# Performance work log

Hardware: AMD Instinct MI355X
Metric: run time of the kernel (lower is better)

## Reference

```python
import jax, jax.numpy as jnp
import numpy as np

N_NODES = 100000
N_EDGES = 3200000
D_IN = 96      # sum(latent_dim)
D_OUT = 32     # latent_dim[-1]
N_HEADS = 4
LEAKY_SLOPE = 0.2


def setup_inputs() -> dict:
    key = jax.random.key(0)
    k_x, k_w, k_a, k_src, k_dst = jax.random.split(key, 5)
    x = jax.random.normal(k_x, (N_NODES, D_IN), dtype=jnp.float32)
    # per-head GAT params (xavier-ish scale)
    W = jax.random.normal(k_w, (N_HEADS, D_IN, D_OUT), dtype=jnp.float32) * (1.414 / np.sqrt(D_IN))
    a = jax.random.normal(k_a, (N_HEADS, 2 * D_OUT), dtype=jnp.float32) * 0.1
    edge_src = jax.random.randint(k_src, (N_EDGES,), 0, N_NODES)
    edge_dst = jax.random.randint(k_dst, (N_EDGES,), 0, N_NODES)
    return {"x": x, "W": W, "a": a, "edge_src": edge_src, "edge_dst": edge_dst}


def reference(x, W, a, edge_src, edge_dst):
    # Multi-head sparse GAT layer (SpGraphAttentionLayer, concat=True, eval mode).
    N = x.shape[0]
    n_heads, _, d_out = W.shape
    outs = []
    for i in range(n_heads):  # small fixed head loop; data dims fully vectorized
        h = x @ W[i]                                   # [N, d_out]
        # a @ cat(h[src], h[dst]) == h[src]@a1 + h[dst]@a2 (avoids [E, 2*d_out] concat)
        s = h[edge_src] @ a[i, :d_out] + h[edge_dst] @ a[i, d_out:]   # [E]
        edge_e = jnp.exp(-jax.nn.leaky_relu(s, LEAKY_SLOPE))          # [E]
        # sparse_coo(edge, edge_e, [N,N]) @ h  ==  scatter-add of edge_e * h[dst] into src
        msg = edge_e[:, None] * h[edge_dst]                           # [E, d_out]
        h_prime = jax.ops.segment_sum(msg, edge_src, num_segments=N)  # [N, d_out]
        outs.append(jax.nn.elu(h_prime))
    return jnp.concatenate(outs, axis=1)  # [N, n_heads * d_out]
```

## Files before the change

### kernel.cpp

```cpp
#include <hip/hip_runtime.h>
#include <hip/hip_bf16.h>

#define DIN 96
#define DOUT 32
#define NH 4
#define DTOT 128
#define SLOPE 0.2f
#define NPBF 64
#define BSH 7
#define BNODES 128
#define MAXB 1024
#define EPB 16384

__device__ __forceinline__ unsigned int packbf2(float lo, float hi) {
    unsigned int a = __float_as_uint(lo), b = __float_as_uint(hi);
    a += 0x7fffu + ((a >> 16) & 1u);
    b += 0x7fffu + ((b >> 16) & 1u);
    return (a >> 16) | (b & 0xffff0000u);
}

__global__ __launch_bounds__(256) void feat_kernel(
    const float* __restrict__ x, const float* __restrict__ W,
    const float* __restrict__ a,
    unsigned int* __restrict__ hq,
    float2* __restrict__ usrc, float2* __restrict__ vdst,
    int* __restrict__ counts, int n_nodes)
{
    __shared__ float Wlo[DIN * 64];
    __shared__ float Whi[DIN * 64];
    __shared__ float al[NH * 2 * DOUT];
    const int t = threadIdx.x;

    if (blockIdx.x == 0)
        for (int i = t; i < MAXB; i += 256) counts[i] = 0;

    for (int i = t; i < DIN * DTOT; i += 256) {
        int k = i >> 7, c = i & 127;
        int head = c >> 5, j = c & 31;
        float w = W[head * (DIN * DOUT) + k * DOUT + j];
        int cbi = c >> 3, jj = c & 7;
        if (jj < 4) Wlo[(k << 6) + (cbi << 2) + jj] = w;
        else        Whi[(k << 6) + (cbi << 2) + (jj - 4)] = w;
    }
    for (int i = t; i < NH * 2 * DOUT; i += 256) al[i] = a[i];
    __syncthreads();

    const int cbi = t & 15;
    const int ng = t >> 4;
    const int node0 = blockIdx.x * NPBF;
    const int g0 = node0 + ng * 4;

    bool ok[4];
    const float* xp[4];
#pragma unroll
    for (int i = 0; i < 4; ++i) {
        ok[i] = (g0 + i) < n_nodes;
        xp[i] = x + (size_t)(g0 + i) * DIN;
    }

    float acc[4][8];
#pragma unroll
    for (int i = 0; i < 4; ++i)
#pragma unroll
        for (int j = 0; j < 8; ++j) acc[i][j] = 0.f;

    for (int k = 0; k < DIN; k += 4) {
        float4 xv[4];
#pragma unroll
        for (int i = 0; i < 4; ++i)
            xv[i] = ok[i] ? *(const float4*)(xp[i] + k)
                          : make_float4(0.f, 0.f, 0.f, 0.f);
#pragma unroll
        for (int kk = 0; kk < 4; ++kk) {
            const float4 wlo = *(const float4*)&Wlo[((k + kk) << 6) + (cbi << 2)];
            const float4 whi = *(const float4*)&Whi[((k + kk) << 6) + (cbi << 2)];
#pragma unroll
            for (int i = 0; i < 4; ++i) {
                const float xvv = (kk == 0) ? xv[i].x : (kk == 1) ? xv[i].y
                                 : (kk == 2) ? xv[i].z : xv[i].w;
                acc[i][0] = fmaf(xvv, wlo.x, acc[i][0]);
                acc[i][1] = fmaf(xvv, wlo.y, acc[i][1]);
                acc[i][2] = fmaf(xvv, wlo.z, acc[i][2]);
                acc[i][3] = fmaf(xvv, wlo.w, acc[i][3]);
                acc[i][4] = fmaf(xvv, whi.x, acc[i][4]);
                acc[i][5] = fmaf(xvv, whi.y, acc[i][5]);
                acc[i][6] = fmaf(xvv, whi.z, acc[i][6]);
                acc[i][7] = fmaf(xvv, whi.w, acc[i][7]);
            }
        }
    }

    const int head = cbi >> 2;
    const int j0 = (cbi & 3) << 3;
#pragma unroll
    for (int i = 0; i < 4; ++i) {
        float ps = 0.f, pd = 0.f;
#pragma unroll
        for (int j = 0; j < 8; ++j) {
            ps += acc[i][j] * al[head * 64 + j0 + j];
            pd += acc[i][j] * al[head * 64 + 32 + j0 + j];
        }
        ps += __shfl_xor(ps, 1); ps += __shfl_xor(ps, 2);
        pd += __shfl_xor(pd, 1); pd += __shfl_xor(pd, 2);
        const int g = g0 + i;
        if (ok[i]) {
            uint4 pk;
            pk.x = packbf2(acc[i][0], acc[i][1]);
            pk.y = packbf2(acc[i][2], acc[i][3]);
            pk.z = packbf2(acc[i][4], acc[i][5]);
            pk.w = packbf2(acc[i][6], acc[i][7]);
            *(uint4*)&hq[(size_t)g * 64 + (cbi << 2)] = pk;
            if ((cbi & 3) == 0) {
                usrc[g * NH + head] = make_float2(__expf(-ps), __expf(-SLOPE * ps));
                vdst[g * NH + head] = make_float2(__expf(-pd), __expf(-SLOPE * pd));
            }
        }
    }
}


__global__ __launch_bounds__(256) void bincount_kernel(
    const int* __restrict__ esrc, int* __restrict__ counts, int n_edges, int nb)
{
    __shared__ int bc[MAXB];
    const int t = threadIdx.x;
    for (int i = t; i < nb; i += 256) bc[i] = 0;
    __syncthreads();
    const int base = blockIdx.x * EPB;
    const int end = min(base + EPB, n_edges);
    for (int e = base + t; e < end; e += 256)
        atomicAdd(&bc[esrc[e] >> BSH], 1);
    __syncthreads();
    for (int i = t; i < nb; i += 256)
        if (bc[i] > 0) atomicAdd(&counts[i], bc[i]);
}

__global__ __launch_bounds__(1024) void bscan_kernel(
    const int* __restrict__ counts, int* __restrict__ bbase,
    int* __restrict__ gcur, int* __restrict__ sbase, int nb)
{
    __shared__ int tmp[1024];
    const int t = threadIdx.x;
    int v = (t < nb) ? counts[t] : 0;
    tmp[t] = v;
    __syncthreads();
    for (int off = 1; off < 1024; off <<= 1) {
        int xv = (t >= off) ? tmp[t - off] : 0;
        __syncthreads();
        tmp[t] += xv;
        __syncthreads();
    }
    if (t < nb) {
        int excl = tmp[t] - v;
        bbase[t] = excl;
        gcur[t] = excl;
        sbase[t] = ((excl + 3) & ~3) + t * (4 * BNODES);
    }
}

__global__ __launch_bounds__(256) void binscatter_kernel(
    const int* __restrict__ esrc, const int* __restrict__ edst,
    int* __restrict__ gcur, unsigned int* __restrict__ binned,
    int n_edges, int nb)
{
    __shared__ int bc[MAXB];
    const int t = threadIdx.x;
    for (int i = t; i < nb; i += 256) bc[i] = 0;
    __syncthreads();
    const int base = blockIdx.x * EPB;
    const int end = min(base + EPB, n_edges);
    for (int e = base + t; e < end; e += 256)
        atomicAdd(&bc[esrc[e] >> BSH], 1);
    __syncthreads();
    for (int i = t; i < nb; i += 256) {
        int c = bc[i];
        bc[i] = (c > 0) ? atomicAdd(&gcur[i], c) : 0;
    }
    __syncthreads();
    for (int e = base + t; e < end; e += 256) {
        int s = esrc[e];
        int pos = atomicAdd(&bc[s >> BSH], 1);
        binned[pos] = ((unsigned int)(s & (BNODES - 1)) << 17) | (unsigned int)edst[e];
    }
}

__global__ __launch_bounds__(256) void binfine_kernel(
    const unsigned int* __restrict__ binned,
    const int* __restrict__ counts, const int* __restrict__ bbase,
    const int* __restrict__ sbase,
    int* __restrict__ offs, int* __restrict__ deg,
    int* __restrict__ slots, int n_nodes)
{
    __shared__ int dcnt[BNODES];
    __shared__ int sc[BNODES];
    __shared__ int dcur[BNODES];
    const int t = threadIdx.x;
    const int b = blockIdx.x;
    const int cnt = counts[b];
    const int start = bbase[b];
    const int sb = sbase[b];
    const int node0 = b << BSH;

    if (t < BNODES) dcnt[t] = 0;
    __syncthreads();
    for (int i = t; i < cnt; i += 256)
        atomicAdd(&dcnt[binned[start + i] >> 17], 1);
    __syncthreads();
    int pd = 0;
    if (t < BNODES) { pd = (dcnt[t] + 3) & ~3; sc[t] = pd; }
    __syncthreads();
    for (int off = 1; off < BNODES; off <<= 1) {
        int v = 0;
        if (t < BNODES && t >= off) v = sc[t - off];
        __syncthreads();
        if (t < BNODES) sc[t] += v;
        __syncthreads();
    }
    if (t < BNODES) {
        int o = sb + sc[t] - pd;
        dcur[t] = o;
        int node = node0 + t;
        if (node < n_nodes) { offs[node] = o; deg[node] = dcnt[t]; }
    }
    __syncthreads();
    for (int i = t; i < cnt; i += 256) {
        unsigned int w = binned[start + i];
        int pos = atomicAdd(&dcur[w >> 17], 1);
        slots[pos] = (int)(w & 0x1ffffu);
    }
}

__global__ __launch_bounds__(256) void gather_kernel(
    const int* __restrict__ slots, const int* __restrict__ offsets,
    const int* __restrict__ deg,
    const unsigned int* __restrict__ hv,
    const float2* __restrict__ usrc, const float2* __restrict__ vdst,
    float* __restrict__ out, int n_nodes)
{
    const int t = threadIdx.x;
    const int node = blockIdx.x * 4 + (t >> 6);
    if (node >= n_nodes) return;
    const int l = t & 63;
    const int head = l >> 4;
    const unsigned loff = (unsigned)l << 2;
    const unsigned hoff = (unsigned)head << 3;
    const char* __restrict__ hvb = (const char*)hv;
    const char* __restrict__ vdb = (const char*)vdst;
    const float2 u = usrc[(unsigned)node * 4u + head];
    const int beg = offsets[node];
    const int d = deg[node];

    float ax0 = 0.f, ay0 = 0.f, ax1 = 0.f, ay1 = 0.f;
    float ax2 = 0.f, ay2 = 0.f, ax3 = 0.f, ay3 = 0.f;

#define LDV(c) (*(const float2*)(vdb + ((((unsigned)(c)) << 5) + hoff)))
#define LDW(c) (*(const unsigned int*)(hvb + ((((unsigned)(c)) << 8) + loff)))
#define COMP(vv, ww, AX, AY) do {                                   \
        float e_ = fminf(u.x * (vv).x, u.y * (vv).y);               \
        AX = fmaf(e_, __uint_as_float((ww) << 16), AX);             \
        AY = fmaf(e_, __uint_as_float((ww) & 0xffff0000u), AY);     \
    } while (0)

    int k = 0;
    if (d >= 4) {
        int4 cA = *(const int4*)(slots + beg);
        float2 vA0 = LDV(cA.x), vA1 = LDV(cA.y), vA2 = LDV(cA.z), vA3 = LDV(cA.w);
        unsigned wA0 = LDW(cA.x), wA1 = LDW(cA.y), wA2 = LDW(cA.z), wA3 = LDW(cA.w);

        for (; k + 12 <= d; k += 8) {
            int4 cB = *(const int4*)(slots + beg + k + 4);
            float2 vB0 = LDV(cB.x), vB1 = LDV(cB.y), vB2 = LDV(cB.z), vB3 = LDV(cB.w);
            unsigned wB0 = LDW(cB.x), wB1 = LDW(cB.y), wB2 = LDW(cB.z), wB3 = LDW(cB.w);
            COMP(vA0, wA0, ax0, ay0); COMP(vA1, wA1, ax1, ay1);
            COMP(vA2, wA2, ax2, ay2); COMP(vA3, wA3, ax3, ay3);
            int4 cN = *(const int4*)(slots + beg + k + 8);
            vA0 = LDV(cN.x); vA1 = LDV(cN.y); vA2 = LDV(cN.z); vA3 = LDV(cN.w);
            wA0 = LDW(cN.x); wA1 = LDW(cN.y); wA2 = LDW(cN.z); wA3 = LDW(cN.w);
            COMP(vB0, wB0, ax0, ay0); COMP(vB1, wB1, ax1, ay1);
            COMP(vB2, wB2, ax2, ay2); COMP(vB3, wB3, ax3, ay3);
        }
        if (k + 8 <= d) {
            int4 cB = *(const int4*)(slots + beg + k + 4);
            float2 vB0 = LDV(cB.x), vB1 = LDV(cB.y), vB2 = LDV(cB.z), vB3 = LDV(cB.w);
            unsigned wB0 = LDW(cB.x), wB1 = LDW(cB.y), wB2 = LDW(cB.z), wB3 = LDW(cB.w);
            COMP(vA0, wA0, ax0, ay0); COMP(vA1, wA1, ax1, ay1);
            COMP(vA2, wA2, ax2, ay2); COMP(vA3, wA3, ax3, ay3);
            COMP(vB0, wB0, ax0, ay0); COMP(vB1, wB1, ax1, ay1);
            COMP(vB2, wB2, ax2, ay2); COMP(vB3, wB3, ax3, ay3);
            k += 8;
        } else {
            COMP(vA0, wA0, ax0, ay0); COMP(vA1, wA1, ax1, ay1);
            COMP(vA2, wA2, ax2, ay2); COMP(vA3, wA3, ax3, ay3);
            k += 4;
        }
    }
    for (; k < d; ++k) {
        int c = slots[beg + k];
        float2 v = LDV(c);
        unsigned w = LDW(c);
        COMP(v, w, ax0, ay0);
    }
#undef LDV
#undef LDW
#undef COMP

    float rx = (ax0 + ax1) + (ax2 + ax3);
    float ry = (ay0 + ay1) + (ay2 + ay3);
    rx = rx > 0.f ? rx : __expf(rx) - 1.f;
    ry = ry > 0.f ? ry : __expf(ry) - 1.f;
    ((float2*)out)[(unsigned)node * 64u + l] = make_float2(rx, ry);
}

extern "C" void kernel_launch(void* const* d_in, const int* in_sizes, int n_in,
                              void* d_out, int out_size, void* d_ws, size_t ws_size,
                              hipStream_t stream)
{
    const float* x  = (const float*)d_in[0];
    const float* W  = (const float*)d_in[1];
    const float* a  = (const float*)d_in[2];
    const int* esrc = (const int*)d_in[3];
    const int* edst = (const int*)d_in[4];
    const int n_nodes = in_sizes[0] / DIN;
    const int n_edges = in_sizes[3];
    float* out = (float*)d_out;

    const int nb = (n_nodes + BNODES - 1) >> BSH;

    unsigned int* hq = (unsigned int*)d_ws;
    float2* usrc = (float2*)(hq + (size_t)n_nodes * 64);
    float2* vdst = usrc + (size_t)n_nodes * NH;
    int* offs   = (int*)(vdst + (size_t)n_nodes * NH);
    int* deg    = offs + n_nodes;
    int* counts = deg + n_nodes;
    int* bbase  = counts + MAXB;
    int* gcur   = bbase + MAXB;
    int* sbase  = gcur + MAXB;
    unsigned int* binned = (unsigned int*)(sbase + MAXB);
    int* slots  = (int*)(binned + n_edges);

    feat_kernel<<<(n_nodes + NPBF - 1) / NPBF, 256, 0, stream>>>(
        x, W, a, hq, usrc, vdst, counts, n_nodes);

    const int binblocks = (n_edges + EPB - 1) / EPB;
    bincount_kernel<<<binblocks, 256, 0, stream>>>(esrc, counts, n_edges, nb);
    bscan_kernel<<<1, 1024, 0, stream>>>(counts, bbase, gcur, sbase, nb);
    binscatter_kernel<<<binblocks, 256, 0, stream>>>(
        esrc, edst, gcur, binned, n_edges, nb);
    binfine_kernel<<<nb, 256, 0, stream>>>(
        binned, counts, bbase, sbase, offs, deg, slots, n_nodes);

    gather_kernel<<<(n_nodes + 3) / 4, 256, 0, stream>>>(
        slots, offs, deg, hq, usrc, vdst, out, n_nodes);
}
```

Measured before the change: 495.4 us.

## Replace two-level binned CSR build with direct global-atomic degree count and scatter

Swaps the bin-count/bin-scatter/bin-fine CSR construction for a simpler pipeline: per-node degree counting via global atomics fused into the feature kernel, a single-block scan over all nodes, and a direct atomic scatter of destinations into per-node slots. This drops two kernels, the intermediate binned buffer and its extra pass over memory. In exchange it relies on 3.2M scattered global atomics to random nodes, and the single-block scan now walks 100k nodes serially per thread. Slot order within a node also becomes nondeterministic.

```diff
diff --git a/kernel.cpp b/kernel.cpp
--- a/kernel.cpp
+++ b/kernel.cpp
@@ -7,10 +7,6 @@
 #define DTOT 128
 #define SLOPE 0.2f
 #define NPBF 64
-#define BSH 7
-#define BNODES 128
-#define MAXB 1024
-#define EPB 16384
 
 __device__ __forceinline__ unsigned int packbf2(float lo, float hi) {
     unsigned int a = __float_as_uint(lo), b = __float_as_uint(hi);
@@ -21,18 +17,24 @@
 
 __global__ __launch_bounds__(256) void feat_kernel(
     const float* __restrict__ x, const float* __restrict__ W,
-    const float* __restrict__ a,
+    const float* __restrict__ a, const int* __restrict__ esrc,
     unsigned int* __restrict__ hq,
     float2* __restrict__ usrc, float2* __restrict__ vdst,
-    int* __restrict__ counts, int n_nodes)
+    int* __restrict__ deg, int n_nodes, int n_edges)
 {
     __shared__ float Wlo[DIN * 64];
     __shared__ float Whi[DIN * 64];
     __shared__ float al[NH * 2 * DOUT];
     const int t = threadIdx.x;
 
-    if (blockIdx.x == 0)
-        for (int i = t; i < MAXB; i += 256) counts[i] = 0;
+    {
+        const int nbk = (int)gridDim.x;
+        const int epbf = (n_edges + nbk - 1) / nbk;
+        const int base = blockIdx.x * epbf;
+        const int end = min(base + epbf, n_edges);
+        for (int e = base + t; e < end; e += 256)
+            atomicAdd(&deg[esrc[e]], 1);
+    }
 
     for (int i = t; i < DIN * DTOT; i += 256) {
         int k = i >> 7, c = i & 127;
@@ -118,115 +120,55 @@
     }
 }
 
-
-__global__ __launch_bounds__(256) void bincount_kernel(
-    const int* __restrict__ esrc, int* __restrict__ counts, int n_edges, int nb)
-{
-    __shared__ int bc[MAXB];
-    const int t = threadIdx.x;
-    for (int i = t; i < nb; i += 256) bc[i] = 0;
-    __syncthreads();
-    const int base = blockIdx.x * EPB;
-    const int end = min(base + EPB, n_edges);
-    for (int e = base + t; e < end; e += 256)
-        atomicAdd(&bc[esrc[e] >> BSH], 1);
-    __syncthreads();
-    for (int i = t; i < nb; i += 256)
-        if (bc[i] > 0) atomicAdd(&counts[i], bc[i]);
-}
-
-__global__ __launch_bounds__(1024) void bscan_kernel(
-    const int* __restrict__ counts, int* __restrict__ bbase,
-    int* __restrict__ gcur, int* __restrict__ sbase, int nb)
+__global__ __launch_bounds__(1024) void scan_kernel(
+    const int* __restrict__ deg, int* __restrict__ offs,
+    int* __restrict__ cur, int n_nodes)
 {
     __shared__ int tmp[1024];
     const int t = threadIdx.x;
-    int v = (t < nb) ? counts[t] : 0;
-    tmp[t] = v;
+    const int C = (n_nodes + 1023) >> 10;
+    const int lo = t * C;
+    const int hi = min(lo + C, n_nodes);
+    int sum = 0;
+    for (int n = lo; n < hi; ++n) sum += (deg[n] + 3) & ~3;
+    tmp[t] = sum;
     __syncthreads();
     for (int off = 1; off < 1024; off <<= 1) {
-        int xv = (t >= off) ? tmp[t - off] : 0;
+        int v = (t >= off) ? tmp[t - off] : 0;
         __syncthreads();
-        tmp[t] += xv;
+        tmp[t] += v;
         __syncthreads();
     }
-    if (t < nb) {
-        int excl = tmp[t] - v;
-        bbase[t] = excl;
-        gcur[t] = excl;
-        sbase[t] = ((excl + 3) & ~3) + t * (4 * BNODES);
-    }
-}
-
-__global__ __launch_bounds__(256) void binscatter_kernel(
+    int run = tmp[t] - sum;
+    for (int n = lo; n < hi; ++n) {
+        offs[n] = run;
+        cur[n] = run;
+        run += (deg[n] + 3) & ~3;
+    }
+}
+
+__global__ __launch_bounds__(256) void scatter_kernel(
     const int* __restrict__ esrc, const int* __restrict__ edst,
-    int* __restrict__ gcur, unsigned int* __restrict__ binned,
-    int n_edges, int nb)
-{
-    __shared__ int bc[MAXB];
-    const int t = threadIdx.x;
-    for (int i = t; i < nb; i += 256) bc[i] = 0;
-    __syncthreads();
-    const int base = blockIdx.x * EPB;
-    const int end = min(base + EPB, n_edges);
-    for (int e = base + t; e < end; e += 256)
-        atomicAdd(&bc[esrc[e] >> BSH], 1);
-    __syncthreads();
-    for (int i = t; i < nb; i += 256) {
-        int c = bc[i];
-        bc[i] = (c > 0) ? atomicAdd(&gcur[i], c) : 0;
-    }
-    __syncthreads();
-    for (int e = base + t; e < end; e += 256) {
-        int s = esrc[e];
-        int pos = atomicAdd(&bc[s >> BSH], 1);
-        binned[pos] = ((unsigned int)(s & (BNODES - 1)) << 17) | (unsigned int)edst[e];
-    }
-}
-
-__global__ __launch_bounds__(256) void binfine_kernel(
-    const unsigned int* __restrict__ binned,
-    const int* __restrict__ counts, const int* __restrict__ bbase,
-    const int* __restrict__ sbase,
-    int* __restrict__ offs, int* __restrict__ deg,
-    int* __restrict__ slots, int n_nodes)
-{
-    __shared__ int dcnt[BNODES];
-    __shared__ int sc[BNODES];
-    __shared__ int dcur[BNODES];
-    const int t = threadIdx.x;
-    const int b = blockIdx.x;
-    const int cnt = counts[b];
-    const int start = bbase[b];
-    const int sb = sbase[b];
-    const int node0 = b << BSH;
-
-    if (t < BNODES) dcnt[t] = 0;
-    __syncthreads();
-    for (int i = t; i < cnt; i += 256)
-        atomicAdd(&dcnt[binned[start + i] >> 17], 1);
-    __syncthreads();
-    int pd = 0;
-    if (t < BNODES) { pd = (dcnt[t] + 3) & ~3; sc[t] = pd; }
-    __syncthreads();
-    for (int off = 1; off < BNODES; off <<= 1) {
-        int v = 0;
-        if (t < BNODES && t >= off) v = sc[t - off];
-        __syncthreads();
-        if (t < BNODES) sc[t] += v;
-        __syncthreads();
-    }
-    if (t < BNODES) {
-        int o = sb + sc[t] - pd;
-        dcur[t] = o;
-        int node = node0 + t;
-        if (node < n_nodes) { offs[node] = o; deg[node] = dcnt[t]; }
-    }
-    __syncthreads();
-    for (int i = t; i < cnt; i += 256) {
-        unsigned int w = binned[start + i];
-        int pos = atomicAdd(&dcur[w >> 17], 1);
-        slots[pos] = (int)(w & 0x1ffffu);
+    int* __restrict__ cur, int* __restrict__ slots, int n_edges)
+{
+    const int nb4 = n_edges >> 2;
+    const int tid = blockIdx.x * 256 + threadIdx.x;
+    const int stride = gridDim.x * 256;
+    for (int i = tid; i < nb4; i += stride) {
+        int4 s4 = ((const int4*)esrc)[i];
+        int4 d4 = ((const int4*)edst)[i];
+        int p0 = atomicAdd(&cur[s4.x], 1);
+        int p1 = atomicAdd(&cur[s4.y], 1);
+        int p2 = atomicAdd(&cur[s4.z], 1);
+        int p3 = atomicAdd(&cur[s4.w], 1);
+        slots[p0] = d4.x;
+        slots[p1] = d4.y;
+        slots[p2] = d4.z;
+        slots[p3] = d4.w;
+    }
+    for (int e = (nb4 << 2) + tid; e < n_edges; e += stride) {
+        int p = atomicAdd(&cur[esrc[e]], 1);
+        slots[p] = edst[e];
     }
 }
 
@@ -324,30 +266,26 @@
     const int n_edges = in_sizes[3];
     float* out = (float*)d_out;
 
-    const int nb = (n_nodes + BNODES - 1) >> BSH;
-
     unsigned int* hq = (unsigned int*)d_ws;
     float2* usrc = (float2*)(hq + (size_t)n_nodes * 64);
     float2* vdst = usrc + (size_t)n_nodes * NH;
     int* offs   = (int*)(vdst + (size_t)n_nodes * NH);
     int* deg    = offs + n_nodes;
-    int* counts = deg + n_nodes;
-    int* bbase  = counts + MAXB;
-    int* gcur   = bbase + MAXB;
-    int* sbase  = gcur + MAXB;
-    unsigned int* binned = (unsigned int*)(sbase + MAXB);
-    int* slots  = (int*)(binned + n_edges);
+    int* cur    = deg + n_nodes;
+    int* slots  = cur + n_nodes;
+
+    hipMemsetAsync(deg, 0, (size_t)n_nodes * sizeof(int), stream);
 
     feat_kernel<<<(n_nodes + NPBF - 1) / NPBF, 256, 0, stream>>>(
-        x, W, a, hq, usrc, vdst, counts, n_nodes);
-
-    const int binblocks = (n_edges + EPB - 1) / EPB;
-    bincount_kernel<<<binblocks, 256, 0, stream>>>(esrc, counts, n_edges, nb);
-    bscan_kernel<<<1, 1024, 0, stream>>>(counts, bbase, gcur, sbase, nb);
-    binscatter_kernel<<<binblocks, 256, 0, stream>>>(
-        esrc, edst, gcur, binned, n_edges, nb);
-    binfine_kernel<<<nb, 256, 0, stream>>>(
-        binned, counts, bbase, sbase, offs, deg, slots, n_nodes);
+        x, W, a, esrc, hq, usrc, vdst, deg, n_nodes, n_edges);
+
+    scan_kernel<<<1, 1024, 0, stream>>>(deg, offs, cur, n_nodes);
+
+    const int nb4 = n_edges >> 2;
+    int sblocks = (nb4 + 255) / 256;
+    if (sblocks > 4096) sblocks = 4096;
+    if (sblocks < 1) sblocks = 1;
+    scatter_kernel<<<sblocks, 256, 0, stream>>>(esrc, edst, cur, slots, n_edges);
 
     gather_kernel<<<(n_nodes + 3) / 4, 256, 0, stream>>>(
         slots, offs, deg, hq, usrc, vdst, out, n_nodes);
```

Result: slower. 991.5 us (+100.2%).

## Fuse bin counting into feature kernel and register-cache edges in binscatter

Applied to the files above, without the earlier changes.

Moves the per-bin edge counting into the feature projection kernel, so one launch and one pass over edge_src disappear; each feature block counts a share of the edges in shared memory. The counts array is now zeroed with hipMemsetAsync, because the fused kernel's blocks all add to it concurrently. binscatter now uses smaller edge chunks (EPB 4096). It loads each thread's 16 src/dst values once with vector int4 loads and keeps them in registers for both the counting and the scatter pass, instead of reading edge arrays twice. This adds shared-memory atomics and an extra shared array to the feature kernel, which may lower its occupancy. The smaller chunks also mean more global atomics on gcur.

```diff
diff --git a/kernel.cpp b/kernel.cpp
--- a/kernel.cpp
+++ b/kernel.cpp
@@ -10,7 +10,7 @@
 #define BSH 7
 #define BNODES 128
 #define MAXB 1024
-#define EPB 16384
+#define EPB 4096
 
 __device__ __forceinline__ unsigned int packbf2(float lo, float hi) {
     unsigned int a = __float_as_uint(lo), b = __float_as_uint(hi);
@@ -21,18 +21,16 @@
 
 __global__ __launch_bounds__(256) void feat_kernel(
     const float* __restrict__ x, const float* __restrict__ W,
-    const float* __restrict__ a,
+    const float* __restrict__ a, const int* __restrict__ esrc,
     unsigned int* __restrict__ hq,
     float2* __restrict__ usrc, float2* __restrict__ vdst,
-    int* __restrict__ counts, int n_nodes)
+    int* __restrict__ counts, int n_nodes, int n_edges, int nb)
 {
     __shared__ float Wlo[DIN * 64];
     __shared__ float Whi[DIN * 64];
     __shared__ float al[NH * 2 * DOUT];
-    const int t = threadIdx.x;
-
-    if (blockIdx.x == 0)
-        for (int i = t; i < MAXB; i += 256) counts[i] = 0;
+    __shared__ int bch[MAXB];
+    const int t = threadIdx.x;
 
     for (int i = t; i < DIN * DTOT; i += 256) {
         int k = i >> 7, c = i & 127;
@@ -43,7 +41,20 @@
         else        Whi[(k << 6) + (cbi << 2) + (jj - 4)] = w;
     }
     for (int i = t; i < NH * 2 * DOUT; i += 256) al[i] = a[i];
-    __syncthreads();
+    for (int i = t; i < MAXB; i += 256) bch[i] = 0;
+    __syncthreads();
+
+    {
+        const int nbk = (int)gridDim.x;
+        const int epbf = (n_edges + nbk - 1) / nbk;
+        const int base = blockIdx.x * epbf;
+        const int end = min(base + epbf, n_edges);
+        for (int e = base + t; e < end; e += 256)
+            atomicAdd(&bch[esrc[e] >> BSH], 1);
+    }
+    __syncthreads();
+    for (int i = t; i < nb; i += 256)
+        if (bch[i] > 0) atomicAdd(&counts[i], bch[i]);
 
     const int cbi = t & 15;
     const int ng = t >> 4;
@@ -118,23 +129,6 @@
     }
 }
 
-
-__global__ __launch_bounds__(256) void bincount_kernel(
-    const int* __restrict__ esrc, int* __restrict__ counts, int n_edges, int nb)
-{
-    __shared__ int bc[MAXB];
-    const int t = threadIdx.x;
-    for (int i = t; i < nb; i += 256) bc[i] = 0;
-    __syncthreads();
-    const int base = blockIdx.x * EPB;
-    const int end = min(base + EPB, n_edges);
-    for (int e = base + t; e < end; e += 256)
-        atomicAdd(&bc[esrc[e] >> BSH], 1);
-    __syncthreads();
-    for (int i = t; i < nb; i += 256)
-        if (bc[i] > 0) atomicAdd(&counts[i], bc[i]);
-}
-
 __global__ __launch_bounds__(1024) void bscan_kernel(
     const int* __restrict__ counts, int* __restrict__ bbase,
     int* __restrict__ gcur, int* __restrict__ sbase, int nb)
@@ -167,20 +161,61 @@
     const int t = threadIdx.x;
     for (int i = t; i < nb; i += 256) bc[i] = 0;
     __syncthreads();
+
     const int base = blockIdx.x * EPB;
     const int end = min(base + EPB, n_edges);
-    for (int e = base + t; e < end; e += 256)
-        atomicAdd(&bc[esrc[e] >> BSH], 1);
-    __syncthreads();
+    const bool full = (end - base) == EPB;
+
+    int se[16], de[16];
+    if (full) {
+        const int4* s4p = (const int4*)(esrc + base);
+        const int4* d4p = (const int4*)(edst + base);
+#pragma unroll
+        for (int j = 0; j < 4; ++j) {
+            int4 s4 = s4p[j * 256 + t];
+            int4 d4 = d4p[j * 256 + t];
+            se[j * 4 + 0] = s4.x; se[j * 4 + 1] = s4.y;
+            se[j * 4 + 2] = s4.z; se[j * 4 + 3] = s4.w;
+            de[j * 4 + 0] = d4.x; de[j * 4 + 1] = d4.y;
+            de[j * 4 + 2] = d4.z; de[j * 4 + 3] = d4.w;
+        }
+#pragma unroll
+        for (int j = 0; j < 16; ++j)
+            atomicAdd(&bc[se[j] >> BSH], 1);
+    } else {
+#pragma unroll
+        for (int j = 0; j < 16; ++j) {
+            const int e = base + j * 256 + t;
+            se[j] = (e < end) ? esrc[e] : 0;
+            de[j] = (e < end) ? edst[e] : 0;
+            if (e < end) atomicAdd(&bc[se[j] >> BSH], 1);
+        }
+    }
+    __syncthreads();
+
     for (int i = t; i < nb; i += 256) {
         int c = bc[i];
         bc[i] = (c > 0) ? atomicAdd(&gcur[i], c) : 0;
     }
     __syncthreads();
-    for (int e = base + t; e < end; e += 256) {
-        int s = esrc[e];
-        int pos = atomicAdd(&bc[s >> BSH], 1);
-        binned[pos] = ((unsigned int)(s & (BNODES - 1)) << 17) | (unsigned int)edst[e];
+
+    if (full) {
+#pragma unroll
+        for (int j = 0; j < 16; ++j) {
+            int s = se[j];
+            int pos = atomicAdd(&bc[s >> BSH], 1);
+            binned[pos] = ((unsigned int)(s & (BNODES - 1)) << 17) | (unsigned int)de[j];
+        }
+    } else {
+#pragma unroll
+        for (int j = 0; j < 16; ++j) {
+            const int e = base + j * 256 + t;
+            if (e < end) {
+                int s = se[j];
+                int pos = atomicAdd(&bc[s >> BSH], 1);
+                binned[pos] = ((unsigned int)(s & (BNODES - 1)) << 17) | (unsigned int)de[j];
+            }
+        }
     }
 }
 
@@ -338,14 +373,16 @@
     unsigned int* binned = (unsigned int*)(sbase + MAXB);
     int* slots  = (int*)(binned + n_edges);
 
+    hipMemsetAsync(counts, 0, MAXB * sizeof(int), stream);
+
     feat_kernel<<<(n_nodes + NPBF - 1) / NPBF, 256, 0, stream>>>(
-        x, W, a, hq, usrc, vdst, counts, n_nodes);
-
-    const int binblocks = (n_edges + EPB - 1) / EPB;
-    bincount_kernel<<<binblocks, 256, 0, stream>>>(esrc, counts, n_edges, nb);
+        x, W, a, esrc, hq, usrc, vdst, counts, n_nodes, n_edges, nb);
+
     bscan_kernel<<<1, 1024, 0, stream>>>(counts, bbase, gcur, sbase, nb);
-    binscatter_kernel<<<binblocks, 256, 0, stream>>>(
+
+    binscatter_kernel<<<(n_edges + EPB - 1) / EPB, 256, 0, stream>>>(
         esrc, edst, gcur, binned, n_edges, nb);
+
     binfine_kernel<<<nb, 256, 0, stream>>>(
         binned, counts, bbase, sbase, offs, deg, slots, n_nodes);
 
```

New measurement: 471.1 us. 1.05x faster.
